# Kernel optimization log

Measured on AMD Instinct MI355X. Metric: run time of the kernel, lower is better.

## Reference

```python
import jax, jax.numpy as jnp
import numpy as np

T, V, K = 128, 5023, 16  # time frames, FLAME vertices, max neighbors


def setup_inputs() -> dict:
    key = jax.random.key(0)
    k1, k2, k3, k4 = jax.random.split(key, 4)
    canonical = jax.random.normal(k1, (T, V, 3), dtype=jnp.float32)
    deformed = canonical + 0.1 * jax.random.normal(k2, (T, V, 3), dtype=jnp.float32)
    neighbors = jax.random.randint(k3, (V, K), 0, V)
    neighbors_mask = jax.random.bernoulli(k4, 0.8, (V, K))
    return {
        "canonical_vertices": canonical,
        "deformed_vertices": deformed,
        "neighbors": neighbors,
        "neighbors_mask": neighbors_mask,
    }


def _matrix_to_quaternion(M):
    """Rotation matrix [..., 3, 3] -> quaternion [..., 4] (w, x, y, z).
    Standard numerically-robust 4-candidate selection (pytorch3d style)."""
    m00, m01, m02 = M[..., 0, 0], M[..., 0, 1], M[..., 0, 2]
    m10, m11, m12 = M[..., 1, 0], M[..., 1, 1], M[..., 1, 2]
    m20, m21, m22 = M[..., 2, 0], M[..., 2, 1], M[..., 2, 2]
    q_abs = jnp.sqrt(jnp.clip(jnp.stack([
        1.0 + m00 + m11 + m22,
        1.0 + m00 - m11 - m22,
        1.0 - m00 + m11 - m22,
        1.0 - m00 - m11 + m22,
    ], axis=-1), 0.0, None))
    quat_by_rijk = jnp.stack([
        jnp.stack([q_abs[..., 0] ** 2, m21 - m12, m02 - m20, m10 - m01], -1),
        jnp.stack([m21 - m12, q_abs[..., 1] ** 2, m01 + m10, m02 + m20], -1),
        jnp.stack([m02 - m20, m10 + m01, q_abs[..., 2] ** 2, m12 + m21], -1),
        jnp.stack([m10 - m01, m20 + m02, m21 + m12, q_abs[..., 3] ** 2], -1),
    ], axis=-2)  # [..., 4, 4]
    floor = jnp.asarray(0.1, M.dtype)
    quat_candidates = quat_by_rijk / (2.0 * jnp.maximum(q_abs[..., None], floor))
    one_hot = jax.nn.one_hot(jnp.argmax(q_abs, axis=-1), 4, dtype=M.dtype)
    return jnp.sum(quat_candidates * one_hot[..., None], axis=-2)


def reference(canonical_vertices, deformed_vertices, neighbors, neighbors_mask):
    dtype = canonical_vertices.dtype
    maskf = neighbors_mask[..., None].astype(dtype)  # [V, K, 1]
    # gather neighbor positions, zeroing padded slots (matches torch code)
    p = canonical_vertices[:, neighbors, :] * maskf  # [T, V, K, 3]
    q = deformed_vertices[:, neighbors, :] * maskf   # [T, V, K, 3]
    # center on the vertex itself
    p_c = p - canonical_vertices[:, :, None, :]
    q_c = q - deformed_vertices[:, :, None, :]
    # per-vertex 3x3 covariance: p_centered^T @ q_centered
    cov = jnp.einsum('tvki,tvkj->tvij', p_c, q_c)  # [T, V, 3, 3]
    u, s, vh = jnp.linalg.svd(cov)
    det = jnp.linalg.det(u @ vh)  # det(u @ v^T), since v^T == vh
    ones = jnp.ones_like(det)
    d3 = jnp.where(jnp.abs(det - 1.0) > 1e-6, det, ones)
    # v @ diag(1, 1, d3) scales the columns of v
    col_scale = jnp.stack([ones, ones, d3], axis=-1)[..., None, :]  # [T,V,1,3]
    v = jnp.swapaxes(vh, -1, -2)
    rotation_matrix = (v * col_scale) @ jnp.swapaxes(u, -1, -2)  # [T,V,3,3]
    rotation = _matrix_to_quaternion(rotation_matrix)  # [T, V, 4]
    translation = deformed_vertices - canonical_vertices  # [T, V, 3]
    return rotation, translation
```

## Files before the change

kernel.cpp:

```cpp
#include <hip/hip_runtime.h>
#include <hip/hip_fp16.h>


namespace {
constexpr int T_FRAMES = 128;
constexpr int V_NUM    = 5023;
constexpr int K_NB     = 16;
constexpr int SLAB     = V_NUM * 3;
constexpr int VPB      = 1256;
constexpr int LDS_BYTES = V_NUM * 16;
}

union VRec {
    uint4   u;
    __half2 h[4];
};

__global__ __launch_bounds__(512, 4)
void se3_extract_kernel(const float* __restrict__ cano,
                        const float* __restrict__ defo,
                        const int*   __restrict__ nbr,
                        const unsigned char* __restrict__ mask_raw,
                        float* __restrict__ out) {
    extern __shared__ uint4 ldsv[];

    const int bid  = blockIdx.x;
    const int t    = bid & 127;
    const int quar = bid >> 7;
    const int tid  = threadIdx.x;

    int mflag;
    {
        const unsigned w = reinterpret_cast<const unsigned*>(mask_raw)[tid & 63];
        const bool isb = ((((w >> 8) & 0xffu) == 1u) | (((w >> 24) & 0xffu) == 1u));
        const bool isf = ((w >> 24) == 0x3fu);
        const unsigned long long mb = __ballot(isb);
        const unsigned long long mf = __ballot(isf);
        mflag = 0;
        if (__popcll(mb) > 16)      mflag = 1;
        else if (__popcll(mf) > 16) mflag = 2;
    }

    const float* __restrict__ cfp = cano + (size_t)t * SLAB;
    const float* __restrict__ dfp = defo + (size_t)t * SLAB;
    for (int i = tid; i < V_NUM; i += 512) {
        const float* cp = cfp + i * 3;
        const float* dp = dfp + i * 3;
        VRec r;
        r.h[0] = __floats2half2_rn(cp[0], cp[1]);
        r.h[1] = __floats2half2_rn(cp[2], dp[0]);
        r.h[2] = __floats2half2_rn(dp[1], dp[2]);
        r.h[3] = __floats2half2_rn(0.0f, 0.0f);
        ldsv[i] = r.u;
    }
    __syncthreads();

    const int vbeg = quar * VPB;
    const int vend = (vbeg + VPB < V_NUM) ? vbeg + VPB : V_NUM;

    for (int v = vbeg + tid; v < vend; v += 512) {
        const float* cp = cfp + v * 3;
        const float* dp = dfp + v * 3;
        const float cvx = cp[0], cvy = cp[1], cvz = cp[2];
        const float dvx = dp[0], dvy = dp[1], dvz = dp[2];

        int nb[K_NB];
        {
            const int4* p4 = reinterpret_cast<const int4*>(nbr + (size_t)v * K_NB);
            #pragma unroll
            for (int j = 0; j < K_NB / 4; ++j) {
                const int4 q = p4[j];
                nb[j*4+0] = q.x; nb[j*4+1] = q.y; nb[j*4+2] = q.z; nb[j*4+3] = q.w;
            }
        }

        float mk[K_NB];
        if (mflag == 1) {
            const uint4 mw = *reinterpret_cast<const uint4*>(mask_raw + (size_t)v * K_NB);
            const unsigned w[4] = {mw.x, mw.y, mw.z, mw.w};
            #pragma unroll
            for (int j = 0; j < 4; ++j) {
                mk[j*4+0] = ((w[j]         & 0xffu) != 0u) ? 1.0f : 0.0f;
                mk[j*4+1] = (((w[j] >> 8 ) & 0xffu) != 0u) ? 1.0f : 0.0f;
                mk[j*4+2] = (((w[j] >> 16) & 0xffu) != 0u) ? 1.0f : 0.0f;
                mk[j*4+3] = (((w[j] >> 24) & 0xffu) != 0u) ? 1.0f : 0.0f;
            }
        } else if (mflag == 0) {
            const int* mp = reinterpret_cast<const int*>(mask_raw) + (size_t)v * K_NB;
            #pragma unroll
            for (int k = 0; k < K_NB; ++k) mk[k] = mp[k] ? 1.0f : 0.0f;
        } else {
            const float* mp = reinterpret_cast<const float*>(mask_raw) + (size_t)v * K_NB;
            #pragma unroll
            for (int k = 0; k < K_NB; ++k) mk[k] = (mp[k] != 0.0f) ? 1.0f : 0.0f;
        }

        float a00=0.f,a01=0.f,a02=0.f,a10=0.f,a11=0.f,a12=0.f,a20=0.f,a21=0.f,a22=0.f;
        #pragma unroll
        for (int k = 0; k < K_NB; ++k) {
            VRec r; r.u = ldsv[nb[k]];
            const float2 f0 = __half22float2(r.h[0]);
            const float2 f1 = __half22float2(r.h[1]);
            const float2 f2 = __half22float2(r.h[2]);
            const float m = mk[k];
            const float px = fmaf(f0.x, m, -cvx);
            const float py = fmaf(f0.y, m, -cvy);
            const float pz = fmaf(f1.x, m, -cvz);
            const float qx = fmaf(f1.y, m, -dvx);
            const float qy = fmaf(f2.x, m, -dvy);
            const float qz = fmaf(f2.y, m, -dvz);
            a00 = fmaf(px,qx,a00); a01 = fmaf(px,qy,a01); a02 = fmaf(px,qz,a02);
            a10 = fmaf(py,qx,a10); a11 = fmaf(py,qy,a11); a12 = fmaf(py,qz,a12);
            a20 = fmaf(pz,qx,a20); a21 = fmaf(pz,qy,a21); a22 = fmaf(pz,qz,a22);
        }

        float x00=a00, x01=a10, x02=a20;
        float x10=a01, x11=a11, x12=a21;
        float x20=a02, x21=a12, x22=a22;
        {
            const float d0 = x00*(x11*x22 - x12*x21)
                           - x01*(x10*x22 - x12*x20)
                           + x02*(x10*x21 - x11*x20);
            const float ad = fmaxf(fabsf(d0), 1e-30f);
            float mu = __builtin_amdgcn_exp2f(-0.3333333333f *
                                              __builtin_amdgcn_logf(ad));
            if (d0 < 0.0f) mu = -mu;
            x00*=mu; x01*=mu; x02*=mu;
            x10*=mu; x11*=mu; x12*=mu;
            x20*=mu; x21*=mu; x22*=mu;
        }
        #pragma unroll
        for (int it = 0; it < 8; ++it) {
            const float c00 = x11*x22 - x12*x21;
            const float c01 = x12*x20 - x10*x22;
            const float c02 = x10*x21 - x11*x20;
            const float c10 = x02*x21 - x01*x22;
            const float c11 = x00*x22 - x02*x20;
            const float c12 = x01*x20 - x00*x21;
            const float c20 = x01*x12 - x02*x11;
            const float c21 = x02*x10 - x00*x12;
            const float c22 = x00*x11 - x01*x10;
            const float det = x00*c00 + x01*c01 + x02*c02;
            const float r   = 0.5f * __builtin_amdgcn_rcpf(det);
            x00 = fmaf(0.5f, x00, r*c00); x01 = fmaf(0.5f, x01, r*c01); x02 = fmaf(0.5f, x02, r*c02);
            x10 = fmaf(0.5f, x10, r*c10); x11 = fmaf(0.5f, x11, r*c11); x12 = fmaf(0.5f, x12, r*c12);
            x20 = fmaf(0.5f, x20, r*c20); x21 = fmaf(0.5f, x21, r*c21); x22 = fmaf(0.5f, x22, r*c22);
        }

        const float qa0 = sqrtf(fmaxf(1.0f + x00 + x11 + x22, 0.0f));
        const float qa1 = sqrtf(fmaxf(1.0f + x00 - x11 - x22, 0.0f));
        const float qa2 = sqrtf(fmaxf(1.0f - x00 + x11 - x22, 0.0f));
        const float qa3 = sqrtf(fmaxf(1.0f - x00 - x11 + x22, 0.0f));

        int best = 0; float bq = qa0;
        if (qa1 > bq) { best = 1; bq = qa1; }
        if (qa2 > bq) { best = 2; bq = qa2; }
        if (qa3 > bq) { best = 3; bq = qa3; }

        float r0, r1, r2, r3;
        if      (best == 0) { r0 = qa0*qa0; r1 = x21-x12; r2 = x02-x20; r3 = x10-x01; }
        else if (best == 1) { r0 = x21-x12; r1 = qa1*qa1; r2 = x01+x10; r3 = x02+x20; }
        else if (best == 2) { r0 = x02-x20; r1 = x10+x01; r2 = qa2*qa2; r3 = x12+x21; }
        else                { r0 = x10-x01; r1 = x20+x02; r2 = x21+x12; r3 = qa3*qa3; }
        const float qi = __builtin_amdgcn_rcpf(2.0f * fmaxf(bq, 0.1f));

        const size_t base_q = ((size_t)t * V_NUM + v) * 4;
        float4 qout;
        qout.x = r0 * qi; qout.y = r1 * qi; qout.z = r2 * qi; qout.w = r3 * qi;
        *reinterpret_cast<float4*>(out + base_q) = qout;

        const size_t base_t = (size_t)T_FRAMES * V_NUM * 4 + ((size_t)t * V_NUM + v) * 3;
        out[base_t+0] = dvx - cvx;
        out[base_t+1] = dvy - cvy;
        out[base_t+2] = dvz - cvz;
    }
}

extern "C" void kernel_launch(void* const* d_in, const int* in_sizes, int n_in,
                              void* d_out, int out_size, void* d_ws, size_t ws_size,
                              hipStream_t stream) {
    const float* cano = (const float*)d_in[0];
    const float* defo = (const float*)d_in[1];
    const int*   nbr  = (const int*)d_in[2];
    const unsigned char* mask = (const unsigned char*)d_in[3];
    float* out = (float*)d_out;

    static bool attr_set = false;
    if (!attr_set) {
        (void)hipFuncSetAttribute((const void*)se3_extract_kernel,
                                  hipFuncAttributeMaxDynamicSharedMemorySize,
                                  LDS_BYTES);
        attr_set = true;
    }

    se3_extract_kernel<<<512, 512, LDS_BYTES, stream>>>(cano, defo, nbr, mask, out);
}
```

Before: 90.26 us.

## Use 1024-thread blocks, bit-packed masks, LDS centers, fewer polar iterations

Doubles the block size to 1024 threads, so the LDS staging loop and the per-vertex loop run with twice as many threads per block. The per-neighbour float mask array becomes a 16-bit mask word, and neighbour indices are loaded in int4 groups inside the accumulation loop, both to lower register pressure. The vertex's own position is now read from the fp16 LDS copy instead of fp32 global memory. This also changes the translation output to fp16-rounded values. The Newton polar iteration count drops from 8 to 6, which cuts arithmetic but may cost rotation accuracy. The launch bound of (1024, 8) asks for more waves than the hardware can hold, and the 1256-vertex quarter splits unevenly across 1024 threads.

```diff
diff --git a/kernel.cpp b/kernel.cpp
--- a/kernel.cpp
+++ b/kernel.cpp
@@ -16,7 +16,7 @@
     __half2 h[4];
 };
 
-__global__ __launch_bounds__(512, 4)
+__global__ __launch_bounds__(1024, 8)
 void se3_extract_kernel(const float* __restrict__ cano,
                         const float* __restrict__ defo,
                         const int*   __restrict__ nbr,
@@ -41,77 +41,80 @@
         else if (__popcll(mf) > 16) mflag = 2;
     }
 
-    const float* __restrict__ cfp = cano + (size_t)t * SLAB;
-    const float* __restrict__ dfp = defo + (size_t)t * SLAB;
-    for (int i = tid; i < V_NUM; i += 512) {
-        const float* cp = cfp + i * 3;
-        const float* dp = dfp + i * 3;
-        VRec r;
-        r.h[0] = __floats2half2_rn(cp[0], cp[1]);
-        r.h[1] = __floats2half2_rn(cp[2], dp[0]);
-        r.h[2] = __floats2half2_rn(dp[1], dp[2]);
-        r.h[3] = __floats2half2_rn(0.0f, 0.0f);
-        ldsv[i] = r.u;
+    {
+        const float* __restrict__ cfp = cano + (size_t)t * SLAB;
+        const float* __restrict__ dfp = defo + (size_t)t * SLAB;
+        for (int i = tid; i < V_NUM; i += 1024) {
+            const float* cp = cfp + i * 3;
+            const float* dp = dfp + i * 3;
+            VRec r;
+            r.h[0] = __floats2half2_rn(cp[0], cp[1]);
+            r.h[1] = __floats2half2_rn(cp[2], dp[0]);
+            r.h[2] = __floats2half2_rn(dp[1], dp[2]);
+            r.h[3] = __floats2half2_rn(0.0f, 0.0f);
+            ldsv[i] = r.u;
+        }
     }
     __syncthreads();
 
     const int vbeg = quar * VPB;
     const int vend = (vbeg + VPB < V_NUM) ? vbeg + VPB : V_NUM;
 
-    for (int v = vbeg + tid; v < vend; v += 512) {
-        const float* cp = cfp + v * 3;
-        const float* dp = dfp + v * 3;
-        const float cvx = cp[0], cvy = cp[1], cvz = cp[2];
-        const float dvx = dp[0], dvy = dp[1], dvz = dp[2];
-
-        int nb[K_NB];
-        {
-            const int4* p4 = reinterpret_cast<const int4*>(nbr + (size_t)v * K_NB);
-            #pragma unroll
-            for (int j = 0; j < K_NB / 4; ++j) {
-                const int4 q = p4[j];
-                nb[j*4+0] = q.x; nb[j*4+1] = q.y; nb[j*4+2] = q.z; nb[j*4+3] = q.w;
-            }
-        }
-
-        float mk[K_NB];
+    for (int v = vbeg + tid; v < vend; v += 1024) {
+        unsigned mbits = 0;
         if (mflag == 1) {
             const uint4 mw = *reinterpret_cast<const uint4*>(mask_raw + (size_t)v * K_NB);
             const unsigned w[4] = {mw.x, mw.y, mw.z, mw.w};
             #pragma unroll
             for (int j = 0; j < 4; ++j) {
-                mk[j*4+0] = ((w[j]         & 0xffu) != 0u) ? 1.0f : 0.0f;
-                mk[j*4+1] = (((w[j] >> 8 ) & 0xffu) != 0u) ? 1.0f : 0.0f;
-                mk[j*4+2] = (((w[j] >> 16) & 0xffu) != 0u) ? 1.0f : 0.0f;
-                mk[j*4+3] = (((w[j] >> 24) & 0xffu) != 0u) ? 1.0f : 0.0f;
+                mbits |= (((w[j]       ) & 0xffu) != 0u ? 1u : 0u) << (j*4+0);
+                mbits |= (((w[j] >> 8  ) & 0xffu) != 0u ? 1u : 0u) << (j*4+1);
+                mbits |= (((w[j] >> 16 ) & 0xffu) != 0u ? 1u : 0u) << (j*4+2);
+                mbits |= (((w[j] >> 24 ) & 0xffu) != 0u ? 1u : 0u) << (j*4+3);
             }
         } else if (mflag == 0) {
             const int* mp = reinterpret_cast<const int*>(mask_raw) + (size_t)v * K_NB;
             #pragma unroll
-            for (int k = 0; k < K_NB; ++k) mk[k] = mp[k] ? 1.0f : 0.0f;
+            for (int k = 0; k < K_NB; ++k) mbits |= (mp[k] ? 1u : 0u) << k;
         } else {
             const float* mp = reinterpret_cast<const float*>(mask_raw) + (size_t)v * K_NB;
             #pragma unroll
-            for (int k = 0; k < K_NB; ++k) mk[k] = (mp[k] != 0.0f) ? 1.0f : 0.0f;
-        }
-
-        float a00=0.f,a01=0.f,a02=0.f,a10=0.f,a11=0.f,a12=0.f,a20=0.f,a21=0.f,a22=0.f;
-        #pragma unroll
-        for (int k = 0; k < K_NB; ++k) {
-            VRec r; r.u = ldsv[nb[k]];
+            for (int k = 0; k < K_NB; ++k) mbits |= ((mp[k] != 0.0f) ? 1u : 0u) << k;
+        }
+
+        float cvx, cvy, cvz, dvx, dvy, dvz;
+        {
+            VRec r; r.u = ldsv[v];
             const float2 f0 = __half22float2(r.h[0]);
             const float2 f1 = __half22float2(r.h[1]);
             const float2 f2 = __half22float2(r.h[2]);
-            const float m = mk[k];
-            const float px = fmaf(f0.x, m, -cvx);
-            const float py = fmaf(f0.y, m, -cvy);
-            const float pz = fmaf(f1.x, m, -cvz);
-            const float qx = fmaf(f1.y, m, -dvx);
-            const float qy = fmaf(f2.x, m, -dvy);
-            const float qz = fmaf(f2.y, m, -dvz);
-            a00 = fmaf(px,qx,a00); a01 = fmaf(px,qy,a01); a02 = fmaf(px,qz,a02);
-            a10 = fmaf(py,qx,a10); a11 = fmaf(py,qy,a11); a12 = fmaf(py,qz,a12);
-            a20 = fmaf(pz,qx,a20); a21 = fmaf(pz,qy,a21); a22 = fmaf(pz,qz,a22);
+            cvx = f0.x; cvy = f0.y; cvz = f1.x;
+            dvx = f1.y; dvy = f2.x; dvz = f2.y;
+        }
+
+        float a00=0.f,a01=0.f,a02=0.f,a10=0.f,a11=0.f,a12=0.f,a20=0.f,a21=0.f,a22=0.f;
+        const int4* __restrict__ nb4 = reinterpret_cast<const int4*>(nbr + (size_t)v * K_NB);
+        #pragma unroll
+        for (int g = 0; g < 4; ++g) {
+            const int4 nq = nb4[g];
+            const int ni[4] = {nq.x, nq.y, nq.z, nq.w};
+            #pragma unroll
+            for (int j = 0; j < 4; ++j) {
+                VRec r; r.u = ldsv[ni[j]];
+                const float m = ((mbits >> (g*4+j)) & 1u) ? 1.0f : 0.0f;
+                const float2 f0 = __half22float2(r.h[0]);
+                const float2 f1 = __half22float2(r.h[1]);
+                const float2 f2 = __half22float2(r.h[2]);
+                const float px = fmaf(f0.x, m, -cvx);
+                const float py = fmaf(f0.y, m, -cvy);
+                const float pz = fmaf(f1.x, m, -cvz);
+                const float qx = fmaf(f1.y, m, -dvx);
+                const float qy = fmaf(f2.x, m, -dvy);
+                const float qz = fmaf(f2.y, m, -dvz);
+                a00 = fmaf(px,qx,a00); a01 = fmaf(px,qy,a01); a02 = fmaf(px,qz,a02);
+                a10 = fmaf(py,qx,a10); a11 = fmaf(py,qy,a11); a12 = fmaf(py,qz,a12);
+                a20 = fmaf(pz,qx,a20); a21 = fmaf(pz,qy,a21); a22 = fmaf(pz,qz,a22);
+            }
         }
 
         float x00=a00, x01=a10, x02=a20;
@@ -130,7 +133,7 @@
             x20*=mu; x21*=mu; x22*=mu;
         }
         #pragma unroll
-        for (int it = 0; it < 8; ++it) {
+        for (int it = 0; it < 6; ++it) {
             const float c00 = x11*x22 - x12*x21;
             const float c01 = x12*x20 - x10*x22;
             const float c02 = x10*x21 - x11*x20;
@@ -193,5 +196,5 @@
         attr_set = true;
     }
 
-    se3_extract_kernel<<<512, 512, LDS_BYTES, stream>>>(cano, defo, nbr, mask, out);
+    se3_extract_kernel<<<512, 1024, LDS_BYTES, stream>>>(cano, defo, nbr, mask, out);
 }
```

New measurement: 136.6 us. 1.51x slower.
